# Optimization experiments

Hardware: AMD Instinct MI355X
Metric: run time of the kernel (lower is better)

## Reference

```python
import jax, jax.numpy as jnp
import numpy as np

TOP_K = 8  # num_experts_per_tok


def setup_inputs() -> dict:
    key = jax.random.key(0)
    k1, k2 = jax.random.split(key)
    hidden_states = jax.random.normal(k1, (4, 4096, 2048), dtype=jnp.float32)
    weight = jax.random.normal(k2, (128, 2048), dtype=jnp.float32) * 0.02
    return {"hidden_states": hidden_states, "weight": weight}


def reference(hidden_states, weight):
    B, S, H = hidden_states.shape
    x = hidden_states.reshape(-1, H).astype(jnp.float32)        # [T, H], T = B*S
    logits = jnp.einsum("th,eh->te", x, weight.astype(jnp.float32))  # [T, E]
    scores = jax.nn.softmax(logits, axis=-1)                    # float32 softmax
    topk_weight, topk_idx = jax.lax.top_k(scores, TOP_K)        # [T, K]
    # norm_topk_prob=True: renormalize selected probabilities
    topk_weight = topk_weight / jnp.sum(topk_weight, axis=-1, keepdims=True)
    return topk_idx, topk_weight
```

## Files before the change

kernel.cpp:

```cpp
#include <hip/hip_runtime.h>
#include <math.h>

#define T_TOKENS 16384
#define HDIM     2048
#define NEXP     128
#define TOPK     8

#define BK    64
#define NCH   (HDIM / BK)
#define TM    32

#define F16_MIN_NORM    6.1035156e-05f
#define SPLIT_SCALE     4096.0f
#define INV_SPLIT_SCALE 2.44140625e-04f

typedef __attribute__((ext_vector_type(8))) _Float16 f16x8;
typedef __attribute__((ext_vector_type(4))) float    f32x4;

#define LGKM0()   asm volatile("s_waitcnt lgkmcnt(0)" ::: "memory")

__device__ __forceinline__ void f16split(float f, _Float16& hi, _Float16& lo) {
    _Float16 h = (_Float16)f;
    float back = (float)h;
    if (fabsf(f) < F16_MIN_NORM) { h = (_Float16)0.f; back = 0.f; }
    lo = (_Float16)((f - back) * SPLIT_SCALE);
    hi = h;
}

__device__ __forceinline__ int swz(int b) {
    return b ^ (((b >> 8) & 3) << 4) ^ (((b >> 11) & 1) << 6);
}

__global__ __launch_bounds__(256) void pack_w(const float* __restrict__ w,
                                              unsigned short* __restrict__ wp1,
                                              unsigned short* __restrict__ wp2) {
    int p = blockIdx.x * 256 + threadIdx.x;
    int lane = p & 63, nt = (p >> 6) & 7, kk = p >> 9;
    int col = lane & 15, quad = lane >> 4;
    const float* src = w + (size_t)(nt * 16 + col) * HDIM + kk * 32 + quad * 8;
    unsigned short h[8], l[8];
#pragma unroll
    for (int j = 0; j < 8; ++j) {
        _Float16 hh, ll;
        f16split(src[j], hh, ll);
        union { _Float16 x; unsigned short u; } ch, cl;
        ch.x = hh; cl.x = ll;
        h[j] = ch.u; l[j] = cl.u;
    }
    *(uint4*)(wp1 + (size_t)p * 8) = *(const uint4*)h;
    *(uint4*)(wp2 + (size_t)p * 8) = *(const uint4*)l;
}

struct BRegs { f16x8 v[8]; };

__global__ __launch_bounds__(256, 2) void moe_gate(const float* __restrict__ x,
                                                   const unsigned short* __restrict__ wp1,
                                                   const unsigned short* __restrict__ wp2,
                                                   float* __restrict__ out_idx,
                                                   float* __restrict__ out_w) {
    __shared__ __align__(16) unsigned char smem[17408];
    float* epil = (float*)smem;

    const int tid  = threadIdx.x;
    const int lane = tid & 63;
    const int wv   = tid >> 6;
    const int col  = lane & 15;
    const int quad = lane >> 4;
    const long tok0 = (long)blockIdx.x * TM;

    const int srow = tid >> 3, skseg = tid & 7;
    const float* xgs = x + (tok0 + srow) * (long)HDIM + skseg * 8;
    const int acell = (((skseg >> 2) * 2 + (srow >> 4)) * 64 + (skseg & 3) * 16 + (srow & 15));
    const int adst  = swz(acell * 16);

    f32x4 acc[2][2], accc[2][2];
#pragma unroll
    for (int m = 0; m < 2; ++m)
#pragma unroll
        for (int j = 0; j < 2; ++j) { acc[m][j] = (f32x4){0,0,0,0}; accc[m][j] = (f32x4){0,0,0,0}; }

    f32x4 Av0, Av1;

    auto loadA = [&](int ch) {
        Av0 = *(const f32x4*)(xgs + ch * BK);
        Av1 = *(const f32x4*)(xgs + ch * BK + 4);
    };
    auto splitWriteA = [&](int b) {
        unsigned short h[8], l[8];
#pragma unroll
        for (int j = 0; j < 8; ++j) {
            _Float16 hh, ll;
            f16split(j < 4 ? Av0[j] : Av1[j - 4], hh, ll);
            union { _Float16 x; unsigned short u; } ch_, cl_;
            ch_.x = hh; cl_.x = ll;
            h[j] = ch_.u; l[j] = cl_.u;
        }
        unsigned char* base = smem + b * 8192;
        *(uint4*)(base + adst)        = *(const uint4*)h;
        *(uint4*)(base + 4096 + adst) = *(const uint4*)l;
    };
    auto loadB = [&](int ch, BRegs& B) {
        const size_t cho = (size_t)ch * 8192;
#pragma unroll
        for (int kk = 0; kk < 2; ++kk)
#pragma unroll
            for (int j = 0; j < 2; ++j) {
                const size_t o = cho + (size_t)(((kk * 8) + (wv * 2 + j)) * 64 + lane) * 8;
                B.v[(kk * 2 + j) * 2 + 0] = *(const f16x8*)(wp1 + o);
                B.v[(kk * 2 + j) * 2 + 1] = *(const f16x8*)(wp2 + o);
            }
    };
    auto mfmaStep = [&](int b, BRegs& B) {
        const unsigned char* base = smem + b * 8192;
#pragma unroll
        for (int kk = 0; kk < 2; ++kk) {
            f16x8 af1v[2], af2v[2];
#pragma unroll
            for (int m = 0; m < 2; ++m) {
                const int bo = swz(((kk * 2 + m) * 64 + lane) * 16);
                af1v[m] = *(const f16x8*)(base + bo);
                af2v[m] = *(const f16x8*)(base + 4096 + bo);
            }
#pragma unroll
            for (int j = 0; j < 2; ++j) {
                f16x8 bf1 = B.v[(kk * 2 + j) * 2 + 0];
                f16x8 bf2 = B.v[(kk * 2 + j) * 2 + 1];
#pragma unroll
                for (int m = 0; m < 2; ++m) {
                    acc[m][j]  = __builtin_amdgcn_mfma_f32_16x16x32_f16(af1v[m], bf1, acc[m][j],  0, 0, 0);
                    accc[m][j] = __builtin_amdgcn_mfma_f32_16x16x32_f16(af1v[m], bf2, accc[m][j], 0, 0, 0);
                    accc[m][j] = __builtin_amdgcn_mfma_f32_16x16x32_f16(af2v[m], bf1, accc[m][j], 0, 0, 0);
                }
            }
        }
    };

    BRegs B0, B1;

    loadA(0);
    loadB(0, B0);
    loadB(1, B1);
    splitWriteA(0);
    loadA(1);
    LGKM0();
    __builtin_amdgcn_s_barrier();

    for (int ch = 0; ch < NCH - 2; ch += 2) {
        splitWriteA(1);
        loadA(ch + 2);
        mfmaStep(0, B0);
        loadB(ch + 2, B0);
        LGKM0();
        __builtin_amdgcn_s_barrier();

        splitWriteA(0);
        loadA(ch + 3);
        mfmaStep(1, B1);
        loadB(ch + 3, B1);
        LGKM0();
        __builtin_amdgcn_s_barrier();
    }
    splitWriteA(1);
    mfmaStep(0, B0);
    LGKM0();
    __builtin_amdgcn_s_barrier();
    mfmaStep(1, B1);
    __syncthreads();

#pragma unroll
    for (int m = 0; m < 2; ++m)
#pragma unroll
        for (int j = 0; j < 2; ++j)
#pragma unroll
            for (int r = 0; r < 4; ++r)
                epil[(m * 16 + quad * 4 + r) * 132 + (wv * 2 + j) * 16 + col] =
                    acc[m][j][r] + accc[m][j][r] * INV_SPLIT_SCALE;
    __syncthreads();

    for (int i = 0; i < 8; ++i) {
        const int t = wv * 8 + i;
        float2 p = *(const float2*)(epil + t * 132 + 2 * lane);
        float v0 = p.x, v1 = p.y;
        const int i0 = 2 * lane, i1 = 2 * lane + 1;

        float topv[TOPK];
        int topi[TOPK];
#pragma unroll
        for (int s = 0; s < TOPK; ++s) {
            float mv = (v0 >= v1) ? v0 : v1;
            int   mi = (v0 >= v1) ? i0 : i1;
#pragma unroll
            for (int off = 32; off >= 1; off >>= 1) {
                float ov = __shfl_xor(mv, off);
                int   oi = __shfl_xor(mi, off);
                if (ov > mv || (ov == mv && oi < mi)) { mv = ov; mi = oi; }
            }
            topv[s] = mv; topi[s] = mi;
            if (i0 == mi) v0 = -INFINITY;
            if (i1 == mi) v1 = -INFINITY;
        }

        const float m = topv[0];
        float sum = 0.f;
#pragma unroll
        for (int s = 0; s < TOPK; ++s) sum += expf(topv[s] - m);
        const float inv = 1.f / sum;

        float myv = topv[0]; int myi = topi[0];
#pragma unroll
        for (int s = 1; s < TOPK; ++s)
            if (lane == s) { myv = topv[s]; myi = topi[s]; }

        if (lane < TOPK) {
            long tok = tok0 + t;
            out_idx[tok * TOPK + lane] = (float)myi;
            out_w[tok * TOPK + lane]   = expf(myv - m) * inv;
        }
    }
}

extern "C" void kernel_launch(void* const* d_in, const int* in_sizes, int n_in,
                              void* d_out, int out_size, void* d_ws, size_t ws_size,
                              hipStream_t stream) {
    const float* x = (const float*)d_in[0];
    const float* w = (const float*)d_in[1];
    float* out = (float*)d_out;

    unsigned short* wp1 = (unsigned short*)d_ws;
    unsigned short* wp2 = wp1 + (size_t)NEXP * HDIM;

    pack_w<<<(64 * 8 * 64) / 256, 256, 0, stream>>>(w, wp1, wp2);
    moe_gate<<<T_TOKENS / TM, 256, 0, stream>>>(x, wp1, wp2, out, out + (size_t)T_TOKENS * TOPK);
}
```

Before: 248.2 us.

## Double K-chunk size to 128 and issue next A load before split-write

Raises the K chunk per pipeline stage from 64 to 128, which doubles the shared A buffers to 32KB and the register-held B fragments to 16 vectors per stage. It also adds two A register sets so the global load for the next chunk is issued before the current chunk's split and LDS write. The goal is to halve the number of barriers and per-chunk overheads and to deepen latency hiding. The cost is much higher register and LDS pressure, which may lower occupancy below the two blocks per CU that the launch bounds request.

```diff
diff --git a/kernel.cpp b/kernel.cpp
--- a/kernel.cpp
+++ b/kernel.cpp
@@ -6,7 +6,7 @@
 #define NEXP     128
 #define TOPK     8
 
-#define BK    64
+#define BK    128
 #define NCH   (HDIM / BK)
 #define TM    32
 
@@ -51,14 +51,15 @@
     *(uint4*)(wp2 + (size_t)p * 8) = *(const uint4*)l;
 }
 
-struct BRegs { f16x8 v[8]; };
+struct ARegs { f32x4 v[4]; };
+struct BRegs { f16x8 v[16]; };
 
 __global__ __launch_bounds__(256, 2) void moe_gate(const float* __restrict__ x,
                                                    const unsigned short* __restrict__ wp1,
                                                    const unsigned short* __restrict__ wp2,
                                                    float* __restrict__ out_idx,
                                                    float* __restrict__ out_w) {
-    __shared__ __align__(16) unsigned char smem[17408];
+    __shared__ __align__(16) unsigned char smem[32768];
     float* epil = (float*)smem;
 
     const int tid  = threadIdx.x;
@@ -70,8 +71,10 @@
 
     const int srow = tid >> 3, skseg = tid & 7;
     const float* xgs = x + (tok0 + srow) * (long)HDIM + skseg * 8;
-    const int acell = (((skseg >> 2) * 2 + (srow >> 4)) * 64 + (skseg & 3) * 16 + (srow & 15));
-    const int adst  = swz(acell * 16);
+    const int g0 = (skseg >> 2) * 2 + (srow >> 4);
+    const int g1 = ((skseg + 8) >> 2) * 2 + (srow >> 4);
+    const int adst0 = swz(g0 * 1024 + (skseg & 3) * 256 + (srow & 15) * 16);
+    const int adst1 = swz(g1 * 1024 + (skseg & 3) * 256 + (srow & 15) * 16);
 
     f32x4 acc[2][2], accc[2][2];
 #pragma unroll
@@ -79,47 +82,53 @@
 #pragma unroll
         for (int j = 0; j < 2; ++j) { acc[m][j] = (f32x4){0,0,0,0}; accc[m][j] = (f32x4){0,0,0,0}; }
 
-    f32x4 Av0, Av1;
-
-    auto loadA = [&](int ch) {
-        Av0 = *(const f32x4*)(xgs + ch * BK);
-        Av1 = *(const f32x4*)(xgs + ch * BK + 4);
-    };
-    auto splitWriteA = [&](int b) {
-        unsigned short h[8], l[8];
+    auto loadA = [&](int ch, ARegs& A) {
+        const float* p = xgs + ch * BK;
+        A.v[0] = *(const f32x4*)(p);
+        A.v[1] = *(const f32x4*)(p + 4);
+        A.v[2] = *(const f32x4*)(p + 64);
+        A.v[3] = *(const f32x4*)(p + 68);
+    };
+    auto splitWriteA = [&](const ARegs& A, int b) {
+        unsigned short h0[8], l0[8], h1[8], l1[8];
 #pragma unroll
         for (int j = 0; j < 8; ++j) {
             _Float16 hh, ll;
-            f16split(j < 4 ? Av0[j] : Av1[j - 4], hh, ll);
+            f16split(j < 4 ? A.v[0][j] : A.v[1][j - 4], hh, ll);
             union { _Float16 x; unsigned short u; } ch_, cl_;
             ch_.x = hh; cl_.x = ll;
-            h[j] = ch_.u; l[j] = cl_.u;
-        }
-        unsigned char* base = smem + b * 8192;
-        *(uint4*)(base + adst)        = *(const uint4*)h;
-        *(uint4*)(base + 4096 + adst) = *(const uint4*)l;
+            h0[j] = ch_.u; l0[j] = cl_.u;
+            f16split(j < 4 ? A.v[2][j] : A.v[3][j - 4], hh, ll);
+            ch_.x = hh; cl_.x = ll;
+            h1[j] = ch_.u; l1[j] = cl_.u;
+        }
+        unsigned char* base = smem + b * 16384;
+        *(uint4*)(base + adst0)        = *(const uint4*)h0;
+        *(uint4*)(base + adst1)        = *(const uint4*)h1;
+        *(uint4*)(base + 8192 + adst0) = *(const uint4*)l0;
+        *(uint4*)(base + 8192 + adst1) = *(const uint4*)l1;
     };
     auto loadB = [&](int ch, BRegs& B) {
-        const size_t cho = (size_t)ch * 8192;
-#pragma unroll
-        for (int kk = 0; kk < 2; ++kk)
+#pragma unroll
+        for (int kk = 0; kk < 4; ++kk)
 #pragma unroll
             for (int j = 0; j < 2; ++j) {
-                const size_t o = cho + (size_t)(((kk * 8) + (wv * 2 + j)) * 64 + lane) * 8;
+                const size_t o = (size_t)(ch * 4 + kk) * 4096
+                               + (size_t)(wv * 2 + j) * 512 + (size_t)lane * 8;
                 B.v[(kk * 2 + j) * 2 + 0] = *(const f16x8*)(wp1 + o);
                 B.v[(kk * 2 + j) * 2 + 1] = *(const f16x8*)(wp2 + o);
             }
     };
-    auto mfmaStep = [&](int b, BRegs& B) {
-        const unsigned char* base = smem + b * 8192;
-#pragma unroll
-        for (int kk = 0; kk < 2; ++kk) {
+    auto mfmaStep = [&](int b, const BRegs& B) {
+        const unsigned char* base = smem + b * 16384;
+#pragma unroll
+        for (int kk = 0; kk < 4; ++kk) {
             f16x8 af1v[2], af2v[2];
 #pragma unroll
             for (int m = 0; m < 2; ++m) {
-                const int bo = swz(((kk * 2 + m) * 64 + lane) * 16);
+                const int bo = swz((kk * 2 + m) * 1024 + lane * 16);
                 af1v[m] = *(const f16x8*)(base + bo);
-                af2v[m] = *(const f16x8*)(base + 4096 + bo);
+                af2v[m] = *(const f16x8*)(base + 8192 + bo);
             }
 #pragma unroll
             for (int j = 0; j < 2; ++j) {
@@ -135,32 +144,33 @@
         }
     };
 
+    ARegs AP, AQ;
     BRegs B0, B1;
 
-    loadA(0);
+    loadA(0, AP);
     loadB(0, B0);
     loadB(1, B1);
-    splitWriteA(0);
-    loadA(1);
+    splitWriteA(AP, 0);
+    loadA(1, AQ);
     LGKM0();
     __builtin_amdgcn_s_barrier();
 
     for (int ch = 0; ch < NCH - 2; ch += 2) {
-        splitWriteA(1);
-        loadA(ch + 2);
+        loadA(ch + 2, AP);
+        splitWriteA(AQ, 1);
         mfmaStep(0, B0);
         loadB(ch + 2, B0);
         LGKM0();
         __builtin_amdgcn_s_barrier();
 
-        splitWriteA(0);
-        loadA(ch + 3);
+        loadA(ch + 3, AQ);
+        splitWriteA(AP, 0);
         mfmaStep(1, B1);
         loadB(ch + 3, B1);
         LGKM0();
         __builtin_amdgcn_s_barrier();
     }
-    splitWriteA(1);
+    splitWriteA(AQ, 1);
     mfmaStep(0, B0);
     LGKM0();
     __builtin_amdgcn_s_barrier();
```

After: 234.3 us. -5.6%, faster.
